# Kernel optimization log

Hardware: AMD Instinct MI355X
Metric: run time of the kernel (lower is better)

## Reference

```python
import jax, jax.numpy as jnp
import numpy as np

B, T, I = 512, 168, 64
H1, H2 = 256, 256


def _lstm_layer(x, W_ih, W_hh, b_ih, b_hh):
    """PyTorch-semantics single-layer LSTM, batch_first, zero init state.
    x: [B,T,in], W_ih: [4H,in], W_hh: [4H,H], biases: [4H]. Gate order i,f,g,o.
    Returns outputs [B,T,H]."""
    H = W_hh.shape[1]
    # Precompute input contribution for all timesteps: [B,T,4H]
    gx_all = jnp.einsum('bti,gi->btg', x, W_ih) + b_ih + b_hh

    def step(carry, gx):
        h, c = carry                      # [B,H] each
        g = gx + h @ W_hh.T               # [B,4H]
        i, f, gg, o = jnp.split(g, 4, axis=-1)
        i = jax.nn.sigmoid(i)
        f = jax.nn.sigmoid(f)
        gg = jnp.tanh(gg)
        o = jax.nn.sigmoid(o)
        c = f * c + i * gg
        h = o * jnp.tanh(c)
        return (h, c), h

    h0 = jnp.zeros((x.shape[0], H), x.dtype)
    (_, _), hs = jax.lax.scan(step, (h0, h0), jnp.swapaxes(gx_all, 0, 1))
    return jnp.swapaxes(hs, 0, 1)         # [B,T,H]


def setup_inputs() -> dict:
    key = jax.random.key(0)
    ks = jax.random.split(key, 9)
    s = 0.05
    return {
        'x_pm':  jax.random.normal(ks[0], (B, T, I), jnp.float32),
        'W_ih1': jax.random.normal(ks[1], (4 * H1, I), jnp.float32) * s,
        'W_hh1': jax.random.normal(ks[2], (4 * H1, H1), jnp.float32) * s,
        'b_ih1': jax.random.normal(ks[3], (4 * H1,), jnp.float32) * s,
        'b_hh1': jax.random.normal(ks[4], (4 * H1,), jnp.float32) * s,
        'W_ih2': jax.random.normal(ks[5], (4 * H2, H1), jnp.float32) * s,
        'W_hh2': jax.random.normal(ks[6], (4 * H2, H2), jnp.float32) * s,
        'b_ih2': jax.random.normal(ks[7], (4 * H2,), jnp.float32) * s,
        'b_hh2': jax.random.normal(ks[8], (4 * H2,), jnp.float32) * s,
    }


def reference(x_pm, W_ih1, W_hh1, b_ih1, b_hh1, W_ih2, W_hh2, b_ih2, b_hh2):
    out1 = _lstm_layer(x_pm, W_ih1, W_hh1, b_ih1, b_hh1)   # [B,T,H1]
    out2 = _lstm_layer(out1, W_ih2, W_hh2, b_ih2, b_hh2)   # [B,T,H2]
    return out2
```

## Files before the change

kernel.cpp:

```cpp
#include <hip/hip_runtime.h>


#define B_ 512
#define T_ 168
#define I_ 64
#define H_ 256

typedef __attribute__((ext_vector_type(8))) short short8;
typedef __attribute__((ext_vector_type(4))) float f32x4;
typedef unsigned short u16;

__device__ __forceinline__ u16 f2bf(float f) {
    unsigned u = __float_as_uint(f);
    return (u16)((u + 0x7fff + ((u >> 16) & 1)) >> 16);
}
__device__ __forceinline__ float bf2f(u16 b) { return __uint_as_float(((unsigned)b) << 16); }

__global__ void prep_w(const float* __restrict__ W_ih, const float* __restrict__ W_hh,
                       const float* __restrict__ b_ih, const float* __restrict__ b_hh,
                       u16* __restrict__ Whi, u16* __restrict__ Wlo, float* __restrict__ BP,
                       int K, int I) {
    int j = blockIdx.y;
    int k = blockIdx.x * 256 + threadIdx.x;
    if (k < K) {
        float v = (k < I) ? W_ih[(size_t)j * I + k] : W_hh[(size_t)j * H_ + (k - I)];
        u16 hi = f2bf(v);
        u16 lo = f2bf(v - bf2f(hi));
        Whi[(size_t)j * K + k] = hi;
        Wlo[(size_t)j * K + k] = lo;
    }
    if (blockIdx.x == 0 && threadIdx.x == 0) BP[j] = b_ih[j] + b_hh[j];
}

__global__ void prep_x(const float* __restrict__ x, u16* __restrict__ Xhi, u16* __restrict__ Xlo, int n) {
    for (int i = blockIdx.x * blockDim.x + threadIdx.x; i < n; i += gridDim.x * blockDim.x) {
        float v = x[i];
        u16 hi = f2bf(v);
        Xhi[i] = hi;
        Xlo[i] = f2bf(v - bf2f(hi));
    }
}

template<int NK, int NK0, bool OUT>
__device__ __forceinline__ void step_body(
    const u16* __restrict__ a0hi, const u16* __restrict__ a0lo, int a0s, long a0base,
    const u16* __restrict__ a1hi, const u16* __restrict__ a1lo,
    u16* __restrict__ hwhi, u16* __restrict__ hwlo,
    float* __restrict__ cbuf,
    const u16* __restrict__ Whi, const u16* __restrict__ Wlo,
    const float* __restrict__ BP, float* __restrict__ outp, int t)
{
    constexpr int K = NK * 32;
    const int lane = threadIdx.x;
    const int b0  = blockIdx.x * 32;
    const int jh0 = blockIdx.y * 16;
    const int lm  = lane & 15;
    const int lk  = (lane >> 4) << 3;

    f32x4 acc[2][4];
#pragma unroll
    for (int m = 0; m < 2; ++m)
#pragma unroll
        for (int g = 0; g < 4; ++g) acc[m][g] = (f32x4){0.f, 0.f, 0.f, 0.f};

    size_t woff = (size_t)(jh0 + lm) * K + lk;

    auto do_k = [&](short8 ah0, short8 al0, short8 ah1, short8 al1) {
#pragma unroll
        for (int g = 0; g < 4; ++g) {
            const size_t wg = woff + (size_t)g * (256 * (size_t)K);
            short8 wh = *(const short8*)(Whi + wg);
            short8 wl = *(const short8*)(Wlo + wg);
            acc[0][g] = __builtin_amdgcn_mfma_f32_16x16x32_bf16(ah0, wh, acc[0][g], 0, 0, 0);
            acc[0][g] = __builtin_amdgcn_mfma_f32_16x16x32_bf16(al0, wh, acc[0][g], 0, 0, 0);
            acc[0][g] = __builtin_amdgcn_mfma_f32_16x16x32_bf16(ah0, wl, acc[0][g], 0, 0, 0);
            acc[1][g] = __builtin_amdgcn_mfma_f32_16x16x32_bf16(ah1, wh, acc[1][g], 0, 0, 0);
            acc[1][g] = __builtin_amdgcn_mfma_f32_16x16x32_bf16(al1, wh, acc[1][g], 0, 0, 0);
            acc[1][g] = __builtin_amdgcn_mfma_f32_16x16x32_bf16(ah1, wl, acc[1][g], 0, 0, 0);
        }
        woff += 32;
    };

    size_t a0off = (size_t)a0base + (size_t)(b0 + lm) * a0s + lk;
#pragma unroll
    for (int ks = 0; ks < NK0; ++ks) {
        short8 ah0 = *(const short8*)(a0hi + a0off);
        short8 al0 = *(const short8*)(a0lo + a0off);
        short8 ah1 = *(const short8*)(a0hi + a0off + (size_t)16 * a0s);
        short8 al1 = *(const short8*)(a0lo + a0off + (size_t)16 * a0s);
        a0off += 32;
        do_k(ah0, al0, ah1, al1);
    }
    size_t a1off = (size_t)(b0 + lm) * H_ + lk;
#pragma unroll 4
    for (int ks = NK0; ks < NK; ++ks) {
        short8 ah0 = *(const short8*)(a1hi + a1off);
        short8 al0 = *(const short8*)(a1lo + a1off);
        short8 ah1 = *(const short8*)(a1hi + a1off + 16 * H_);
        short8 al1 = *(const short8*)(a1lo + a1off + 16 * H_);
        a1off += 32;
        do_k(ah0, al0, ah1, al1);
    }

    const int jh = jh0 + lm;
    const float bi = BP[jh], bf = BP[256 + jh], bg = BP[512 + jh], bo = BP[768 + jh];
#pragma unroll
    for (int m = 0; m < 2; ++m) {
#pragma unroll
        for (int i = 0; i < 4; ++i) {
            const int b = b0 + m * 16 + ((lane >> 4) << 2) + i;
            float gi = acc[m][0][i] + bi;
            float gf = acc[m][1][i] + bf;
            float gg = acc[m][2][i] + bg;
            float go = acc[m][3][i] + bo;
            float si = 1.f / (1.f + __expf(-gi));
            float sf = 1.f / (1.f + __expf(-gf));
            float tg = tanhf(gg);
            float so = 1.f / (1.f + __expf(-go));
            const size_t ci = (size_t)b * H_ + jh;
            float cn = sf * cbuf[ci] + si * tg;
            cbuf[ci] = cn;
            float h = so * tanhf(cn);
            u16 hh = f2bf(h);
            hwhi[ci] = hh;
            hwlo[ci] = f2bf(h - bf2f(hh));
            if (OUT) outp[((size_t)b * T_ + t) * H_ + jh] = h;
        }
    }
}

struct StepArgs {
    const u16 *x_hi, *x_lo;
    const u16 *h1r_hi, *h1r_lo;
    u16 *h1w_hi, *h1w_lo;
    const u16 *h2r_hi, *h2r_lo;
    u16 *h2w_hi, *h2w_lo;
    float *c1, *c2;
    const u16 *W1hi, *W1lo, *W2hi, *W2lo;
    const float *BP1, *BP2;
    float *out;
    int t1, t2;
};

__global__ __launch_bounds__(64) void lstm_step_k(StepArgs a) {
    if (blockIdx.z == 0) {
        if (a.t1 >= T_) return;
        step_body<10, 2, false>(a.x_hi, a.x_lo, T_ * I_, (long)a.t1 * I_,
                                a.h1r_hi, a.h1r_lo, a.h1w_hi, a.h1w_lo, a.c1,
                                a.W1hi, a.W1lo, a.BP1, nullptr, 0);
    } else {
        if (a.t2 < 0) return;
        step_body<16, 8, true>(a.h1r_hi, a.h1r_lo, H_, 0,
                               a.h2r_hi, a.h2r_lo, a.h2w_hi, a.h2w_lo, a.c2,
                               a.W2hi, a.W2lo, a.BP2, a.out, a.t2);
    }
}

extern "C" void kernel_launch(void* const* d_in, const int* in_sizes, int n_in,
                              void* d_out, int out_size, void* d_ws, size_t ws_size,
                              hipStream_t stream) {
    const float* x     = (const float*)d_in[0];
    const float* W_ih1 = (const float*)d_in[1];
    const float* W_hh1 = (const float*)d_in[2];
    const float* b_ih1 = (const float*)d_in[3];
    const float* b_hh1 = (const float*)d_in[4];
    const float* W_ih2 = (const float*)d_in[5];
    const float* W_hh2 = (const float*)d_in[6];
    const float* b_ih2 = (const float*)d_in[7];
    const float* b_hh2 = (const float*)d_in[8];
    (void)in_sizes; (void)n_in; (void)out_size; (void)ws_size;

    size_t off = 0;
    char* base = (char*)d_ws;
    auto alloc = [&](size_t bytes) { void* p = base + off; off = (off + bytes + 255) & ~(size_t)255; return p; };

    const int K1 = I_ + H_;
    const int K2 = H_ + H_;
    u16* W1hi = (u16*)alloc((size_t)1024 * K1 * 2);
    u16* W1lo = (u16*)alloc((size_t)1024 * K1 * 2);
    u16* W2hi = (u16*)alloc((size_t)1024 * K2 * 2);
    u16* W2lo = (u16*)alloc((size_t)1024 * K2 * 2);
    float* BP1 = (float*)alloc(1024 * 4);
    float* BP2 = (float*)alloc(1024 * 4);
    u16* Xhi = (u16*)alloc((size_t)B_ * T_ * I_ * 2);
    u16* Xlo = (u16*)alloc((size_t)B_ * T_ * I_ * 2);

    char* state0 = (char*)alloc(0);
    const size_t HB = (size_t)B_ * H_ * 2;
    u16* H1hi[2] = {(u16*)alloc(HB), (u16*)alloc(HB)};
    u16* H1lo[2] = {(u16*)alloc(HB), (u16*)alloc(HB)};
    u16* H2hi[2] = {(u16*)alloc(HB), (u16*)alloc(HB)};
    u16* H2lo[2] = {(u16*)alloc(HB), (u16*)alloc(HB)};
    float* C1 = (float*)alloc((size_t)B_ * H_ * 4);
    float* C2 = (float*)alloc((size_t)B_ * H_ * 4);
    size_t stateBytes = (char*)base + off - state0;

    hipMemsetAsync(state0, 0, stateBytes, stream);
    prep_w<<<dim3(2, 1024), 256, 0, stream>>>(W_ih1, W_hh1, b_ih1, b_hh1, W1hi, W1lo, BP1, K1, I_);
    prep_w<<<dim3(2, 1024), 256, 0, stream>>>(W_ih2, W_hh2, b_ih2, b_hh2, W2hi, W2lo, BP2, K2, H_);
    prep_x<<<2048, 256, 0, stream>>>(x, Xhi, Xlo, B_ * T_ * I_);

    dim3 grid(B_ / 32, H_ / 16, 2);
    for (int s = 0; s <= T_; ++s) {
        const int t1 = s, t2 = s - 1;
        const int wp1 = t1 & 1, rp1 = wp1 ^ 1;
        const int wp2 = (t2 >= 0) ? (t2 & 1) : 0, rp2 = wp2 ^ 1;
        StepArgs a;
        a.x_hi = Xhi; a.x_lo = Xlo;
        a.h1r_hi = H1hi[rp1]; a.h1r_lo = H1lo[rp1];
        a.h1w_hi = H1hi[wp1]; a.h1w_lo = H1lo[wp1];
        a.h2r_hi = H2hi[rp2]; a.h2r_lo = H2lo[rp2];
        a.h2w_hi = H2hi[wp2]; a.h2w_lo = H2lo[wp2];
        a.c1 = C1; a.c2 = C2;
        a.W1hi = W1hi; a.W1lo = W1lo; a.W2hi = W2hi; a.W2lo = W2lo;
        a.BP1 = BP1; a.BP2 = BP2;
        a.out = (float*)d_out;
        a.t1 = t1; a.t2 = t2;
        lstm_step_k<<<grid, 64, 0, stream>>>(a);
    }
}
```

Before: 3.214 ms.

## Replace per-timestep launches with a persistent cooperative kernel and grid barrier

Measured after the change: 5.698 ms. 77.3% more time.

```diff
diff --git a/kernel.cpp b/kernel.cpp
--- a/kernel.cpp
+++ b/kernel.cpp
@@ -5,6 +5,7 @@
 #define T_ 168
 #define I_ 64
 #define H_ 256
+#define NBLK 256
 
 typedef __attribute__((ext_vector_type(8))) short short8;
 typedef __attribute__((ext_vector_type(4))) float f32x4;
@@ -15,6 +16,12 @@
     return (u16)((u + 0x7fff + ((u >> 16) & 1)) >> 16);
 }
 __device__ __forceinline__ float bf2f(u16 b) { return __uint_as_float(((unsigned)b) << 16); }
+__device__ __forceinline__ float sigm(float x) { return 1.f / (1.f + __expf(-x)); }
+__device__ __forceinline__ float tanh_c(float x) {
+    float xc = fminf(fmaxf(x, -15.f), 15.f);
+    float e = __expf(2.f * xc);
+    return (e - 1.f) / (e + 1.f);
+}
 
 __global__ void prep_w(const float* __restrict__ W_ih, const float* __restrict__ W_hh,
                        const float* __restrict__ b_ih, const float* __restrict__ b_hh,
@@ -25,134 +32,143 @@
     if (k < K) {
         float v = (k < I) ? W_ih[(size_t)j * I + k] : W_hh[(size_t)j * H_ + (k - I)];
         u16 hi = f2bf(v);
-        u16 lo = f2bf(v - bf2f(hi));
         Whi[(size_t)j * K + k] = hi;
-        Wlo[(size_t)j * K + k] = lo;
+        Wlo[(size_t)j * K + k] = f2bf(v - bf2f(hi));
     }
     if (blockIdx.x == 0 && threadIdx.x == 0) BP[j] = b_ih[j] + b_hh[j];
 }
 
-__global__ void prep_x(const float* __restrict__ x, u16* __restrict__ Xhi, u16* __restrict__ Xlo, int n) {
-    for (int i = blockIdx.x * blockDim.x + threadIdx.x; i < n; i += gridDim.x * blockDim.x) {
-        float v = x[i];
+__global__ void prep_x_t(const float* __restrict__ x, u16* __restrict__ Xhi, u16* __restrict__ Xlo) {
+    int n = B_ * T_ * I_;
+    for (int idx = blockIdx.x * blockDim.x + threadIdx.x; idx < n; idx += gridDim.x * blockDim.x) {
+        float v = x[idx];
+        int i = idx & 63, bt = idx >> 6;
+        int t = bt % T_, b = bt / T_;
+        size_t o = ((size_t)t * B_ + b) * I_ + i;
         u16 hi = f2bf(v);
-        Xhi[i] = hi;
-        Xlo[i] = f2bf(v - bf2f(hi));
+        Xhi[o] = hi;
+        Xlo[o] = f2bf(v - bf2f(hi));
     }
 }
 
-template<int NK, int NK0, bool OUT>
-__device__ __forceinline__ void step_body(
-    const u16* __restrict__ a0hi, const u16* __restrict__ a0lo, int a0s, long a0base,
-    const u16* __restrict__ a1hi, const u16* __restrict__ a1lo,
-    u16* __restrict__ hwhi, u16* __restrict__ hwlo,
-    float* __restrict__ cbuf,
-    const u16* __restrict__ Whi, const u16* __restrict__ Wlo,
-    const float* __restrict__ BP, float* __restrict__ outp, int t)
-{
-    constexpr int K = NK * 32;
-    const int lane = threadIdx.x;
-    const int b0  = blockIdx.x * 32;
-    const int jh0 = blockIdx.y * 16;
-    const int lm  = lane & 15;
-    const int lk  = (lane >> 4) << 3;
-
-    f32x4 acc[2][4];
-#pragma unroll
-    for (int m = 0; m < 2; ++m)
-#pragma unroll
-        for (int g = 0; g < 4; ++g) acc[m][g] = (f32x4){0.f, 0.f, 0.f, 0.f};
-
-    size_t woff = (size_t)(jh0 + lm) * K + lk;
-
-    auto do_k = [&](short8 ah0, short8 al0, short8 ah1, short8 al1) {
-#pragma unroll
-        for (int g = 0; g < 4; ++g) {
-            const size_t wg = woff + (size_t)g * (256 * (size_t)K);
-            short8 wh = *(const short8*)(Whi + wg);
-            short8 wl = *(const short8*)(Wlo + wg);
-            acc[0][g] = __builtin_amdgcn_mfma_f32_16x16x32_bf16(ah0, wh, acc[0][g], 0, 0, 0);
-            acc[0][g] = __builtin_amdgcn_mfma_f32_16x16x32_bf16(al0, wh, acc[0][g], 0, 0, 0);
-            acc[0][g] = __builtin_amdgcn_mfma_f32_16x16x32_bf16(ah0, wl, acc[0][g], 0, 0, 0);
-            acc[1][g] = __builtin_amdgcn_mfma_f32_16x16x32_bf16(ah1, wh, acc[1][g], 0, 0, 0);
-            acc[1][g] = __builtin_amdgcn_mfma_f32_16x16x32_bf16(al1, wh, acc[1][g], 0, 0, 0);
-            acc[1][g] = __builtin_amdgcn_mfma_f32_16x16x32_bf16(ah1, wl, acc[1][g], 0, 0, 0);
-        }
-        woff += 32;
-    };
-
-    size_t a0off = (size_t)a0base + (size_t)(b0 + lm) * a0s + lk;
-#pragma unroll
-    for (int ks = 0; ks < NK0; ++ks) {
-        short8 ah0 = *(const short8*)(a0hi + a0off);
-        short8 al0 = *(const short8*)(a0lo + a0off);
-        short8 ah1 = *(const short8*)(a0hi + a0off + (size_t)16 * a0s);
-        short8 al1 = *(const short8*)(a0lo + a0off + (size_t)16 * a0s);
-        a0off += 32;
-        do_k(ah0, al0, ah1, al1);
-    }
-    size_t a1off = (size_t)(b0 + lm) * H_ + lk;
-#pragma unroll 4
-    for (int ks = NK0; ks < NK; ++ks) {
-        short8 ah0 = *(const short8*)(a1hi + a1off);
-        short8 al0 = *(const short8*)(a1lo + a1off);
-        short8 ah1 = *(const short8*)(a1hi + a1off + 16 * H_);
-        short8 al1 = *(const short8*)(a1lo + a1off + 16 * H_);
-        a1off += 32;
-        do_k(ah0, al0, ah1, al1);
-    }
-
-    const int jh = jh0 + lm;
-    const float bi = BP[jh], bf = BP[256 + jh], bg = BP[512 + jh], bo = BP[768 + jh];
-#pragma unroll
-    for (int m = 0; m < 2; ++m) {
-#pragma unroll
-        for (int i = 0; i < 4; ++i) {
-            const int b = b0 + m * 16 + ((lane >> 4) << 2) + i;
-            float gi = acc[m][0][i] + bi;
-            float gf = acc[m][1][i] + bf;
-            float gg = acc[m][2][i] + bg;
-            float go = acc[m][3][i] + bo;
-            float si = 1.f / (1.f + __expf(-gi));
-            float sf = 1.f / (1.f + __expf(-gf));
-            float tg = tanhf(gg);
-            float so = 1.f / (1.f + __expf(-go));
-            const size_t ci = (size_t)b * H_ + jh;
-            float cn = sf * cbuf[ci] + si * tg;
-            cbuf[ci] = cn;
-            float h = so * tanhf(cn);
-            u16 hh = f2bf(h);
-            hwhi[ci] = hh;
-            hwlo[ci] = f2bf(h - bf2f(hh));
-            if (OUT) outp[((size_t)b * T_ + t) * H_ + jh] = h;
-        }
-    }
-}
-
-struct StepArgs {
-    const u16 *x_hi, *x_lo;
-    const u16 *h1r_hi, *h1r_lo;
-    u16 *h1w_hi, *h1w_lo;
-    const u16 *h2r_hi, *h2r_lo;
-    u16 *h2w_hi, *h2w_lo;
-    float *c1, *c2;
+struct PArgs {
+    const u16 *Xhi, *Xlo;
+    u16 *H1hi[2], *H1lo[2], *H2hi[2], *H2lo[2];
+    float *C1, *C2;
     const u16 *W1hi, *W1lo, *W2hi, *W2lo;
     const float *BP1, *BP2;
     float *out;
-    int t1, t2;
+    unsigned *bar;
 };
 
-__global__ __launch_bounds__(64) void lstm_step_k(StepArgs a) {
-    if (blockIdx.z == 0) {
-        if (a.t1 >= T_) return;
-        step_body<10, 2, false>(a.x_hi, a.x_lo, T_ * I_, (long)a.t1 * I_,
-                                a.h1r_hi, a.h1r_lo, a.h1w_hi, a.h1w_lo, a.c1,
-                                a.W1hi, a.W1lo, a.BP1, nullptr, 0);
-    } else {
-        if (a.t2 < 0) return;
-        step_body<16, 8, true>(a.h1r_hi, a.h1r_lo, H_, 0,
-                               a.h2r_hi, a.h2r_lo, a.h2w_hi, a.h2w_lo, a.c2,
-                               a.W2hi, a.W2lo, a.BP2, a.out, a.t2);
+__global__ __launch_bounds__(256, 1) void lstm_persist(PArgs a) {
+    const int blk = blockIdx.x;
+    const bool isL1 = blk >= 128;
+    const int sub = isL1 ? (blk - 128) : blk;
+    const int bg  = sub & 7;
+    const int jh0 = (sub >> 3) << 4;
+    const int lane = threadIdx.x & 63;
+    const int wave = threadIdx.x >> 6;
+    const int lm   = lane & 15;
+    const int lk8  = (lane >> 4) << 3;
+    const int b0   = bg * 64 + wave * 16;
+    const int jh   = jh0 + lm;
+    const int K    = isL1 ? (I_ + H_) : (2 * H_);
+
+    const u16* Whi = isL1 ? a.W1hi : a.W2hi;
+    const u16* Wlo = isL1 ? a.W1lo : a.W2lo;
+    const float* BP = isL1 ? a.BP1 : a.BP2;
+    float* C = isL1 ? a.C1 : a.C2;
+
+    const size_t w0 = (size_t)(0 * H_ + jh) * K + lk8;
+    const size_t w1 = (size_t)(1 * H_ + jh) * K + lk8;
+    const size_t w2 = (size_t)(2 * H_ + jh) * K + lk8;
+    const size_t w3 = (size_t)(3 * H_ + jh) * K + lk8;
+    const float bi_ = BP[jh], bf_ = BP[H_ + jh], bg_ = BP[2 * H_ + jh], bo_ = BP[3 * H_ + jh];
+    const size_t arow = (size_t)(b0 + lm);
+
+    for (int s = 0; s <= T_; ++s) {
+        const int t = isL1 ? s : (s - 1);
+        const bool active = isL1 ? (t < T_) : (t >= 0);
+        if (active) {
+            f32x4 acc0 = {0.f,0.f,0.f,0.f}, acc1 = acc0, acc2 = acc0, acc3 = acc0;
+            auto DOK = [&](short8 ah, short8 al, int k) {
+                short8 wh, wl;
+                wh = *(const short8*)(Whi + w0 + k); wl = *(const short8*)(Wlo + w0 + k);
+                acc0 = __builtin_amdgcn_mfma_f32_16x16x32_bf16(ah, wh, acc0, 0, 0, 0);
+                acc0 = __builtin_amdgcn_mfma_f32_16x16x32_bf16(al, wh, acc0, 0, 0, 0);
+                acc0 = __builtin_amdgcn_mfma_f32_16x16x32_bf16(ah, wl, acc0, 0, 0, 0);
+                wh = *(const short8*)(Whi + w1 + k); wl = *(const short8*)(Wlo + w1 + k);
+                acc1 = __builtin_amdgcn_mfma_f32_16x16x32_bf16(ah, wh, acc1, 0, 0, 0);
+                acc1 = __builtin_amdgcn_mfma_f32_16x16x32_bf16(al, wh, acc1, 0, 0, 0);
+                acc1 = __builtin_amdgcn_mfma_f32_16x16x32_bf16(ah, wl, acc1, 0, 0, 0);
+                wh = *(const short8*)(Whi + w2 + k); wl = *(const short8*)(Wlo + w2 + k);
+                acc2 = __builtin_amdgcn_mfma_f32_16x16x32_bf16(ah, wh, acc2, 0, 0, 0);
+                acc2 = __builtin_amdgcn_mfma_f32_16x16x32_bf16(al, wh, acc2, 0, 0, 0);
+                acc2 = __builtin_amdgcn_mfma_f32_16x16x32_bf16(ah, wl, acc2, 0, 0, 0);
+                wh = *(const short8*)(Whi + w3 + k); wl = *(const short8*)(Wlo + w3 + k);
+                acc3 = __builtin_amdgcn_mfma_f32_16x16x32_bf16(ah, wh, acc3, 0, 0, 0);
+                acc3 = __builtin_amdgcn_mfma_f32_16x16x32_bf16(al, wh, acc3, 0, 0, 0);
+                acc3 = __builtin_amdgcn_mfma_f32_16x16x32_bf16(ah, wl, acc3, 0, 0, 0);
+            };
+            if (isL1) {
+                const u16* xh = a.Xhi + ((size_t)t * B_ + b0 + lm) * I_ + lk8;
+                const u16* xl = a.Xlo + ((size_t)t * B_ + b0 + lm) * I_ + lk8;
+#pragma unroll
+                for (int ks = 0; ks < 2; ++ks)
+                    DOK(*(const short8*)(xh + ks * 32), *(const short8*)(xl + ks * 32), ks * 32);
+                const int rp = (t & 1) ^ 1;
+                const u16* hh = a.H1hi[rp] + arow * H_ + lk8;
+                const u16* hl = a.H1lo[rp] + arow * H_ + lk8;
+#pragma unroll 4
+                for (int ks = 0; ks < 8; ++ks)
+                    DOK(*(const short8*)(hh + ks * 32), *(const short8*)(hl + ks * 32), I_ + ks * 32);
+            } else {
+                const int p1 = t & 1;
+                const u16* hh = a.H1hi[p1] + arow * H_ + lk8;
+                const u16* hl = a.H1lo[p1] + arow * H_ + lk8;
+#pragma unroll 4
+                for (int ks = 0; ks < 8; ++ks)
+                    DOK(*(const short8*)(hh + ks * 32), *(const short8*)(hl + ks * 32), ks * 32);
+                const int rp2 = p1 ^ 1;
+                const u16* gh = a.H2hi[rp2] + arow * H_ + lk8;
+                const u16* gl = a.H2lo[rp2] + arow * H_ + lk8;
+#pragma unroll 4
+                for (int ks = 0; ks < 8; ++ks)
+                    DOK(*(const short8*)(gh + ks * 32), *(const short8*)(gl + ks * 32), H_ + ks * 32);
+            }
+            const int wp = t & 1;
+            u16* ohi = isL1 ? a.H1hi[wp] : a.H2hi[wp];
+            u16* olo = isL1 ? a.H1lo[wp] : a.H2lo[wp];
+#pragma unroll
+            for (int i = 0; i < 4; ++i) {
+                const int b = b0 + ((lane >> 4) << 2) + i;
+                float gi = acc0[i] + bi_;
+                float gf = acc1[i] + bf_;
+                float gg = acc2[i] + bg_;
+                float go = acc3[i] + bo_;
+                float si = sigm(gi), sf = sigm(gf), tg = tanh_c(gg), so = sigm(go);
+                const size_t ci = (size_t)b * H_ + jh;
+                float cn = sf * C[ci] + si * tg;
+                C[ci] = cn;
+                float h = so * tanh_c(cn);
+                u16 h16 = f2bf(h);
+                ohi[ci] = h16;
+                olo[ci] = f2bf(h - bf2f(h16));
+                if (!isL1) a.out[((size_t)b * T_ + t) * H_ + jh] = h;
+            }
+        }
+        if (s < T_) {
+            __syncthreads();
+            if (threadIdx.x == 0) {
+                __hip_atomic_fetch_add(a.bar, 1u, __ATOMIC_RELEASE, __HIP_MEMORY_SCOPE_AGENT);
+                const unsigned target = (unsigned)(s + 1) * NBLK;
+                while (__hip_atomic_load(a.bar, __ATOMIC_RELAXED, __HIP_MEMORY_SCOPE_AGENT) < target)
+                    __builtin_amdgcn_s_sleep(4);
+                __builtin_amdgcn_fence(__ATOMIC_ACQUIRE, "agent");
+            }
+            __syncthreads();
+        }
     }
 }
 
@@ -175,7 +191,7 @@
     auto alloc = [&](size_t bytes) { void* p = base + off; off = (off + bytes + 255) & ~(size_t)255; return p; };
 
     const int K1 = I_ + H_;
-    const int K2 = H_ + H_;
+    const int K2 = 2 * H_;
     u16* W1hi = (u16*)alloc((size_t)1024 * K1 * 2);
     u16* W1lo = (u16*)alloc((size_t)1024 * K1 * 2);
     u16* W2hi = (u16*)alloc((size_t)1024 * K2 * 2);
@@ -185,37 +201,29 @@
     u16* Xhi = (u16*)alloc((size_t)B_ * T_ * I_ * 2);
     u16* Xlo = (u16*)alloc((size_t)B_ * T_ * I_ * 2);
 
-    char* state0 = (char*)alloc(0);
+    char* state0 = base + off;
+    unsigned* bar = (unsigned*)alloc(256);
     const size_t HB = (size_t)B_ * H_ * 2;
-    u16* H1hi[2] = {(u16*)alloc(HB), (u16*)alloc(HB)};
-    u16* H1lo[2] = {(u16*)alloc(HB), (u16*)alloc(HB)};
-    u16* H2hi[2] = {(u16*)alloc(HB), (u16*)alloc(HB)};
-    u16* H2lo[2] = {(u16*)alloc(HB), (u16*)alloc(HB)};
-    float* C1 = (float*)alloc((size_t)B_ * H_ * 4);
-    float* C2 = (float*)alloc((size_t)B_ * H_ * 4);
-    size_t stateBytes = (char*)base + off - state0;
+    PArgs pa;
+    pa.H1hi[0] = (u16*)alloc(HB); pa.H1hi[1] = (u16*)alloc(HB);
+    pa.H1lo[0] = (u16*)alloc(HB); pa.H1lo[1] = (u16*)alloc(HB);
+    pa.H2hi[0] = (u16*)alloc(HB); pa.H2hi[1] = (u16*)alloc(HB);
+    pa.H2lo[0] = (u16*)alloc(HB); pa.H2lo[1] = (u16*)alloc(HB);
+    pa.C1 = (float*)alloc((size_t)B_ * H_ * 4);
+    pa.C2 = (float*)alloc((size_t)B_ * H_ * 4);
+    size_t stateBytes = (size_t)((base + off) - state0);
 
     hipMemsetAsync(state0, 0, stateBytes, stream);
     prep_w<<<dim3(2, 1024), 256, 0, stream>>>(W_ih1, W_hh1, b_ih1, b_hh1, W1hi, W1lo, BP1, K1, I_);
     prep_w<<<dim3(2, 1024), 256, 0, stream>>>(W_ih2, W_hh2, b_ih2, b_hh2, W2hi, W2lo, BP2, K2, H_);
-    prep_x<<<2048, 256, 0, stream>>>(x, Xhi, Xlo, B_ * T_ * I_);
-
-    dim3 grid(B_ / 32, H_ / 16, 2);
-    for (int s = 0; s <= T_; ++s) {
-        const int t1 = s, t2 = s - 1;
-        const int wp1 = t1 & 1, rp1 = wp1 ^ 1;
-        const int wp2 = (t2 >= 0) ? (t2 & 1) : 0, rp2 = wp2 ^ 1;
-        StepArgs a;
-        a.x_hi = Xhi; a.x_lo = Xlo;
-        a.h1r_hi = H1hi[rp1]; a.h1r_lo = H1lo[rp1];
-        a.h1w_hi = H1hi[wp1]; a.h1w_lo = H1lo[wp1];
-        a.h2r_hi = H2hi[rp2]; a.h2r_lo = H2lo[rp2];
-        a.h2w_hi = H2hi[wp2]; a.h2w_lo = H2lo[wp2];
-        a.c1 = C1; a.c2 = C2;
-        a.W1hi = W1hi; a.W1lo = W1lo; a.W2hi = W2hi; a.W2lo = W2lo;
-        a.BP1 = BP1; a.BP2 = BP2;
-        a.out = (float*)d_out;
-        a.t1 = t1; a.t2 = t2;
-        lstm_step_k<<<grid, 64, 0, stream>>>(a);
-    }
-}
+    prep_x_t<<<512, 256, 0, stream>>>(x, Xhi, Xlo);
+
+    pa.Xhi = Xhi; pa.Xlo = Xlo;
+    pa.W1hi = W1hi; pa.W1lo = W1lo; pa.W2hi = W2hi; pa.W2lo = W2lo;
+    pa.BP1 = BP1; pa.BP2 = BP2;
+    pa.out = (float*)d_out;
+    pa.bar = bar;
+
+    void* kp[] = {(void*)&pa};
+    hipLaunchCooperativeKernel((const void*)lstm_persist, dim3(NBLK), dim3(256), kp, 0, stream);
+}
```
